# Optimization experiments

Measured on AMD Instinct MI355X. Metric: run time of the kernel, lower is better.

## Reference

```python
import jax, jax.numpy as jnp
import numpy as np

N_HEAD = 16

def setup_inputs() -> dict:
    key = jax.random.key(0)
    ks = jax.random.split(key, 4)
    B, S, E = 2, 2048, 1024
    x = jax.random.normal(ks[0], (B, S, E), dtype=jnp.float32)
    W_qkv = jax.random.normal(ks[1], (E, 3 * E), dtype=jnp.float32) * (1.0 / np.sqrt(E))
    b_qkv = jnp.zeros((3 * E,), dtype=jnp.float32)
    W_proj = jax.random.normal(ks[2], (E, E), dtype=jnp.float32) * (1.0 / np.sqrt(E))
    b_proj = jnp.zeros((E,), dtype=jnp.float32)
    return {"x": x, "W_qkv": W_qkv, "b_qkv": b_qkv, "W_proj": W_proj, "b_proj": b_proj}


def reference(x, W_qkv, b_qkv, W_proj, b_proj):
    B, S, E = x.shape
    H = N_HEAD
    D = E // H
    scale = 1.0 / np.sqrt(D).astype(np.float32)

    qkv = x @ W_qkv + b_qkv                      # [B,S,3E]
    q, k, v = jnp.split(qkv, 3, axis=2)
    # Original code does .view(B, H, S, D) directly (no transpose); replicate exactly.
    q = q.reshape(B, H, S, D)
    k = k.reshape(B, H, S, D)
    v = v.reshape(B, H, S, D)

    att = jnp.einsum('bhqd,bhkd->bhqk', q, k) * scale   # [B,H,S,S]
    causal = jnp.tril(jnp.ones((S, S), dtype=bool))      # True = visible
    att = jnp.where(causal[None, None], att, jnp.float32(-jnp.inf))
    att = jax.nn.softmax(att, axis=-1)
    # dropout is identity in eval mode (p used only at train)
    res = jnp.einsum('bhqk,bhkd->bhqd', att, v)           # [B,H,S,D]
    res = res.transpose(0, 2, 1, 3).reshape(B, S, E)      # matches transpose(1,2).view
    return res @ W_proj + b_proj
```

## Files before the change

### kernel.cpp

```cpp
#include <hip/hip_runtime.h>
#include <hip/hip_bf16.h>

using bf16 = __hip_bfloat16;
using s16x8 = __attribute__((ext_vector_type(8))) short;
using f32x4 = __attribute__((ext_vector_type(4))) float;
typedef unsigned short u16;
typedef unsigned int u32;

#define DEVINL __device__ __forceinline__

DEVINL u16 f2bf(float f) {
  u32 u = __float_as_uint(f);
  u32 r = (u + 0x7fffu + ((u >> 16) & 1u)) >> 16;
  return (u16)r;
}

DEVINL void gload_lds16(const void* g, void* l) {
  __builtin_amdgcn_global_load_lds(
      (__attribute__((address_space(1))) void*)(void*)(g),
      (__attribute__((address_space(3))) void*)(l), 16, 0, 0);
}

__global__ __launch_bounds__(256) void cast_f32_bf16(
    const float* __restrict__ in, bf16* __restrict__ out, int n) {
  int i = (blockIdx.x * 256 + threadIdx.x) * 8;
  float4 a = *(const float4*)(in + i);
  float4 b = *(const float4*)(in + i + 4);
  u16 tmp[8] = {f2bf(a.x), f2bf(a.y), f2bf(a.z), f2bf(a.w),
                f2bf(b.x), f2bf(b.y), f2bf(b.z), f2bf(b.w)};
  *(uint4*)(out + i) = *(const uint4*)tmp;
}

__global__ __launch_bounds__(256) void transpose_cast(
    const float* __restrict__ W, bf16* __restrict__ Wt, int K, int N) {
  __shared__ float tile[64][65];
  int n0 = blockIdx.x * 64, k0 = blockIdx.y * 64;
  int t = threadIdx.x;
#pragma unroll
  for (int i = 0; i < 16; ++i) {
    int idx = i * 256 + t;
    int r = idx >> 6, c = idx & 63;
    tile[r][c] = W[(size_t)(k0 + r) * N + n0 + c];
  }
  __syncthreads();
#pragma unroll
  for (int i = 0; i < 16; ++i) {
    int idx = i * 256 + t;
    int r = idx >> 6, c = idx & 63;
    Wt[(size_t)(n0 + r) * K + k0 + c] = __float2bfloat16(tile[c][r]);
  }
}

template <int MODE>
__global__ __launch_bounds__(256) void gemm_bt(
    const bf16* __restrict__ A, const bf16* __restrict__ Bt,
    const float* __restrict__ bias,
    bf16* __restrict__ q, bf16* __restrict__ k, bf16* __restrict__ v,
    float* __restrict__ outf, int M, int N, int K) {
  __shared__ bf16 As[128 * 64];
  __shared__ bf16 Bs[128 * 64];
  const int tid = threadIdx.x;
  const int w = tid >> 6, lane = tid & 63;
  const int lr = lane >> 4, lc = lane & 15;
  const int wr = w >> 1, wc = w & 1;
  const int m0 = blockIdx.x * 128, n0 = blockIdx.y * 128;

  f32x4 acc[4][4] = {};

  const int srow = lane >> 3;
  const int scolb = ((lane & 7) * 16) ^ (srow << 4);
  const char* Abase = (const char*)(A + (size_t)m0 * K);
  const char* Bbase = (const char*)(Bt + (size_t)n0 * K);
  const int Krow = K * 2;

  for (int kt = 0; kt < K; kt += 64) {
    __syncthreads();
#pragma unroll
    for (int c = 0; c < 4; ++c) {
      int row = w * 32 + c * 8 + srow;
      gload_lds16(Abase + (size_t)row * Krow + kt * 2 + scolb,
                  (char*)As + w * 4096 + c * 1024 + lane * 16);
    }
#pragma unroll
    for (int c = 0; c < 4; ++c) {
      int row = w * 32 + c * 8 + srow;
      gload_lds16(Bbase + (size_t)row * Krow + kt * 2 + scolb,
                  (char*)Bs + w * 4096 + c * 1024 + lane * 16);
    }
    __syncthreads();
#pragma unroll
    for (int ks = 0; ks < 2; ++ks) {
      s16x8 af[4], bfr[4];
#pragma unroll
      for (int mi = 0; mi < 4; ++mi) {
        int row = wr * 64 + mi * 16 + lc;
        int colb = (ks * 64 + lr * 16) ^ ((row & 7) << 4);
        af[mi] = *(const s16x8*)((const char*)As + row * 128 + colb);
      }
#pragma unroll
      for (int ni = 0; ni < 4; ++ni) {
        int row = wc * 64 + ni * 16 + lc;
        int colb = (ks * 64 + lr * 16) ^ ((row & 7) << 4);
        bfr[ni] = *(const s16x8*)((const char*)Bs + row * 128 + colb);
      }
#pragma unroll
      for (int mi = 0; mi < 4; ++mi)
#pragma unroll
        for (int ni = 0; ni < 4; ++ni)
          acc[mi][ni] = __builtin_amdgcn_mfma_f32_16x16x32_bf16(
              af[mi], bfr[ni], acc[mi][ni], 0, 0, 0);
    }
  }

#pragma unroll
  for (int mi = 0; mi < 4; ++mi) {
#pragma unroll
    for (int ni = 0; ni < 4; ++ni) {
      int col = n0 + wc * 64 + ni * 16 + lc;
      float bb = bias[col];
      int rowb = m0 + wr * 64 + mi * 16 + lr * 4;
#pragma unroll
      for (int r = 0; r < 4; ++r) {
        float val = acc[mi][ni][r] + bb;
        int row = rowb + r;
        if (MODE == 0) {
          bf16* o = (col < 1024) ? q : ((col < 2048) ? k : v);
          int cc = col & 1023;
          o[(size_t)row * 1024 + cc] = __float2bfloat16(val);
        } else {
          outf[(size_t)row * N + col] = val;
        }
      }
    }
  }
}

__global__ __launch_bounds__(256) void attn_kernel(
    const bf16* __restrict__ qb, const bf16* __restrict__ kb,
    const bf16* __restrict__ vb, bf16* __restrict__ ob) {
  __shared__ bf16 Ks[64 * 64];
  __shared__ bf16 Vt[64 * 64];
  __shared__ bf16 Ps[128 * 64];

  const int idx = blockIdx.x;
  const int qt = 15 - (idx >> 5);
  const int bh = idx & 31;
  const int b = bh >> 4, h = bh & 15;
  const size_t hb = ((size_t)(b * 2048 + h * 128)) * 1024;
  const bf16* qh = qb + hb;
  const bf16* kh = kb + hb;
  const bf16* vh = vb + hb;

  const int tid = threadIdx.x;
  const int w = tid >> 6, lane = tid & 63;
  const int lr = lane >> 4, lc = lane & 15;

  s16x8 qf[2][2];
#pragma unroll
  for (int mi = 0; mi < 2; ++mi)
#pragma unroll
    for (int ks = 0; ks < 2; ++ks)
      qf[mi][ks] = *(const s16x8*)(qh + (size_t)(qt * 128 + w * 32 + mi * 16 + lc) * 64 +
                                   ks * 32 + lr * 8);

  f32x4 o_acc[2][4] = {};
  float m_run[2][4], l_run[2][4];
#pragma unroll
  for (int mi = 0; mi < 2; ++mi)
#pragma unroll
    for (int r = 0; r < 4; ++r) { m_run[mi][r] = -INFINITY; l_run[mi][r] = 0.f; }

  const int srow = lane >> 3;
  const int scolb = ((lane & 7) * 16) ^ (srow << 4);

  const int nt = (qt + 1) * 2;
  for (int t = 0; t < nt; ++t) {
    __syncthreads();
#pragma unroll
    for (int c = 0; c < 2; ++c) {
      int row = w * 16 + c * 8 + srow;
      gload_lds16((const char*)(kh + (size_t)(t * 64 + row) * 64) + scolb,
                  (char*)Ks + w * 2048 + c * 1024 + lane * 16);
    }
#pragma unroll
    for (int c = 0; c < 2; ++c) {
      int key = lane;
      int d0 = (c * 4 + w) * 8;
      uint4 val = *(const uint4*)(vh + (size_t)(t * 64 + key) * 64 + d0);
      const u16* e = (const u16*)&val;
#pragma unroll
      for (int j = 0; j < 8; ++j) {
        int d = d0 + j;
        *(u16*)((char*)Vt + d * 128 + ((key * 2) ^ ((j & 7) << 4))) = e[j];
      }
    }
    __syncthreads();

    f32x4 s[2][4] = {};
#pragma unroll
    for (int ks = 0; ks < 2; ++ks) {
      s16x8 kf[4];
#pragma unroll
      for (int nj = 0; nj < 4; ++nj) {
        int row = nj * 16 + lc;
        int colb = (ks * 64 + lr * 16) ^ ((row & 7) << 4);
        kf[nj] = *(const s16x8*)((const char*)Ks + row * 128 + colb);
      }
#pragma unroll
      for (int mi = 0; mi < 2; ++mi)
#pragma unroll
        for (int nj = 0; nj < 4; ++nj)
          s[mi][nj] = __builtin_amdgcn_mfma_f32_16x16x32_bf16(
              qf[mi][ks], kf[nj], s[mi][nj], 0, 0, 0);
    }

#pragma unroll
    for (int mi = 0; mi < 2; ++mi) {
#pragma unroll
      for (int r = 0; r < 4; ++r) {
        const int qlocal = w * 32 + mi * 16 + lr * 4 + r;
        const int qg = qt * 128 + qlocal;
        float vv[4];
        float mx = -INFINITY;
#pragma unroll
        for (int nj = 0; nj < 4; ++nj) {
          int kg = t * 64 + nj * 16 + lc;
          float val = s[mi][nj][r] * 0.125f;
          val = (kg <= qg) ? val : -INFINITY;
          vv[nj] = val;
          mx = fmaxf(mx, val);
        }
#pragma unroll
        for (int off = 1; off < 16; off <<= 1) mx = fmaxf(mx, __shfl_xor(mx, off));
        float mold = m_run[mi][r];
        float mnew = fmaxf(mold, mx);
        float sf = __expf(mold - mnew);
        m_run[mi][r] = mnew;
        float ps = 0.f;
#pragma unroll
        for (int nj = 0; nj < 4; ++nj) {
          float p = __expf(vv[nj] - mnew);
          ps += p;
          int key = nj * 16 + lc;
          *(u16*)((char*)Ps + qlocal * 128 + ((key * 2) ^ ((qlocal & 7) << 4))) = f2bf(p);
        }
#pragma unroll
        for (int off = 1; off < 16; off <<= 1) ps += __shfl_xor(ps, off);
        l_run[mi][r] = l_run[mi][r] * sf + ps;
#pragma unroll
        for (int dj = 0; dj < 4; ++dj) o_acc[mi][dj][r] *= sf;
      }
    }

#pragma unroll
    for (int ks = 0; ks < 2; ++ks) {
      s16x8 pf[2], vf[4];
#pragma unroll
      for (int mi = 0; mi < 2; ++mi) {
        int row = w * 32 + mi * 16 + lc;
        int colb = (ks * 64 + lr * 16) ^ ((row & 7) << 4);
        pf[mi] = *(const s16x8*)((const char*)Ps + row * 128 + colb);
      }
#pragma unroll
      for (int dj = 0; dj < 4; ++dj) {
        int row = dj * 16 + lc;
        int colb = (ks * 64 + lr * 16) ^ ((row & 7) << 4);
        vf[dj] = *(const s16x8*)((const char*)Vt + row * 128 + colb);
      }
#pragma unroll
      for (int mi = 0; mi < 2; ++mi)
#pragma unroll
        for (int dj = 0; dj < 4; ++dj)
          o_acc[mi][dj] = __builtin_amdgcn_mfma_f32_16x16x32_bf16(
              pf[mi], vf[dj], o_acc[mi][dj], 0, 0, 0);
    }
  }

#pragma unroll
  for (int mi = 0; mi < 2; ++mi) {
#pragma unroll
    for (int r = 0; r < 4; ++r) {
      float inv = 1.0f / l_run[mi][r];
      int qg = qt * 128 + w * 32 + mi * 16 + lr * 4 + r;
      size_t base = ((size_t)(b * 2048 + qg)) * 1024 + h * 64;
#pragma unroll
      for (int dj = 0; dj < 4; ++dj)
        ob[base + dj * 16 + lc] = __float2bfloat16(o_acc[mi][dj][r] * inv);
    }
  }
}

extern "C" void kernel_launch(void* const* d_in, const int* in_sizes, int n_in,
                              void* d_out, int out_size, void* d_ws, size_t ws_size,
                              hipStream_t stream) {
  const float* x = (const float*)d_in[0];
  const float* Wqkv = (const float*)d_in[1];
  const float* bqkv = (const float*)d_in[2];
  const float* Wproj = (const float*)d_in[3];
  const float* bproj = (const float*)d_in[4];
  float* out = (float*)d_out;

  char* ws = (char*)d_ws;
  bf16* xb = (bf16*)(ws);
  bf16* Wt1 = (bf16*)(ws + 8388608);
  bf16* Wt2 = (bf16*)(ws + 14680064);
  bf16* qb = (bf16*)(ws + 16777216);
  bf16* kb = (bf16*)(ws + 25165824);
  bf16* vb = (bf16*)(ws + 33554432);
  bf16* Ob = xb;

  cast_f32_bf16<<<2048, 256, 0, stream>>>(x, xb, 4096 * 1024);
  transpose_cast<<<dim3(48, 16), 256, 0, stream>>>(Wqkv, Wt1, 1024, 3072);
  transpose_cast<<<dim3(16, 16), 256, 0, stream>>>(Wproj, Wt2, 1024, 1024);
  gemm_bt<0><<<dim3(32, 24), 256, 0, stream>>>(xb, Wt1, bqkv, qb, kb, vb, nullptr,
                                               4096, 3072, 1024);
  attn_kernel<<<512, 256, 0, stream>>>(qb, kb, vb, Ob);
  gemm_bt<1><<<dim3(32, 8), 256, 0, stream>>>(Ob, Wt2, bproj, nullptr, nullptr, nullptr,
                                              out, 4096, 1024, 1024);
}
```

Baseline: 247.9 us.

## Rewrite attention with 32x32 MFMA, register-resident P, and pre-transposed V

```diff
diff --git a/kernel.cpp b/kernel.cpp
--- a/kernel.cpp
+++ b/kernel.cpp
@@ -4,6 +4,7 @@
 using bf16 = __hip_bfloat16;
 using s16x8 = __attribute__((ext_vector_type(8))) short;
 using f32x4 = __attribute__((ext_vector_type(4))) float;
+using f32x16 = __attribute__((ext_vector_type(16))) float;
 typedef unsigned short u16;
 typedef unsigned int u32;
 
@@ -13,6 +14,13 @@
   u32 u = __float_as_uint(f);
   u32 r = (u + 0x7fffu + ((u >> 16) & 1u)) >> 16;
   return (u16)r;
+}
+
+DEVINL u32 pkbf(float a, float b) {
+  __hip_bfloat162 h = __float22bfloat162_rn(make_float2(a, b));
+  union { __hip_bfloat162 h; u32 u; } c;
+  c.h = h;
+  return c.u;
 }
 
 DEVINL void gload_lds16(const void* g, void* l) {
@@ -48,6 +56,34 @@
     int idx = i * 256 + t;
     int r = idx >> 6, c = idx & 63;
     Wt[(size_t)(n0 + r) * K + k0 + c] = __float2bfloat16(tile[c][r]);
+  }
+}
+
+__global__ __launch_bounds__(256) void v_transpose(
+    const bf16* __restrict__ vb, bf16* __restrict__ vt) {
+  __shared__ u16 lt[64][68];
+  const int bh = blockIdx.y;
+  const int s0 = blockIdx.x * 64;
+  const int tid = threadIdx.x;
+  const bf16* src = vb + (size_t)bh * 131072;
+#pragma unroll
+  for (int i = 0; i < 2; ++i) {
+    int c = i * 256 + tid;
+    int srow = c >> 3, sc = (c & 7) * 8;
+    uint4 v = *(const uint4*)(src + (size_t)(s0 + srow) * 64 + sc);
+    const u16* e = (const u16*)&v;
+#pragma unroll
+    for (int j = 0; j < 8; ++j) lt[srow][sc + j] = e[j];
+  }
+  __syncthreads();
+#pragma unroll
+  for (int i = 0; i < 2; ++i) {
+    int c = i * 256 + tid;
+    int drow = c >> 3, sc = (c & 7) * 8;
+    u16 tmp[8];
+#pragma unroll
+    for (int j = 0; j < 8; ++j) tmp[j] = lt[sc + j][drow];
+    *(uint4*)(vt + (size_t)(bh * 64 + drow) * 2048 + s0 + sc) = *(const uint4*)tmp;
   }
 }
 
@@ -124,6 +160,7 @@
         float val = acc[mi][ni][r] + bb;
         int row = rowb + r;
         if (MODE == 0) {
+          if (col < 1024) val *= 0.125f;
           bf16* o = (col < 1024) ? q : ((col < 2048) ? k : v);
           int cc = col & 1023;
           o[(size_t)row * 1024 + cc] = __float2bfloat16(val);
@@ -137,156 +174,144 @@
 
 __global__ __launch_bounds__(256) void attn_kernel(
     const bf16* __restrict__ qb, const bf16* __restrict__ kb,
-    const bf16* __restrict__ vb, bf16* __restrict__ ob) {
-  __shared__ bf16 Ks[64 * 64];
-  __shared__ bf16 Vt[64 * 64];
-  __shared__ bf16 Ps[128 * 64];
-
+    const bf16* __restrict__ vtp, bf16* __restrict__ ob) {
   const int idx = blockIdx.x;
-  const int qt = 15 - (idx >> 5);
-  const int bh = idx & 31;
+  const int bh_lo = idx & 7;
+  const int r0 = idx >> 3;
+  const int bh = ((r0 >> 4) << 3) + bh_lo;
+  const int qbk = 15 - (r0 & 15);
   const int b = bh >> 4, h = bh & 15;
-  const size_t hb = ((size_t)(b * 2048 + h * 128)) * 1024;
+  const int tid = threadIdx.x;
+  const int w = tid >> 6;
+  const int lane = tid & 63;
+  const int l31 = lane & 31;
+  const int hi = lane >> 5;
+
+  const int jj = qbk * 4 + w;
+  const int qbase = jj * 32;
+  const int qg = qbase + l31;
+
+  const size_t hb = (size_t)bh * 131072;
   const bf16* qh = qb + hb;
   const bf16* kh = kb + hb;
-  const bf16* vh = vb + hb;
-
-  const int tid = threadIdx.x;
-  const int w = tid >> 6, lane = tid & 63;
-  const int lr = lane >> 4, lc = lane & 15;
-
-  s16x8 qf[2][2];
-#pragma unroll
-  for (int mi = 0; mi < 2; ++mi)
-#pragma unroll
-    for (int ks = 0; ks < 2; ++ks)
-      qf[mi][ks] = *(const s16x8*)(qh + (size_t)(qt * 128 + w * 32 + mi * 16 + lc) * 64 +
-                                   ks * 32 + lr * 8);
-
-  f32x4 o_acc[2][4] = {};
-  float m_run[2][4], l_run[2][4];
-#pragma unroll
-  for (int mi = 0; mi < 2; ++mi)
-#pragma unroll
-    for (int r = 0; r < 4; ++r) { m_run[mi][r] = -INFINITY; l_run[mi][r] = 0.f; }
-
-  const int srow = lane >> 3;
-  const int scolb = ((lane & 7) * 16) ^ (srow << 4);
-
-  const int nt = (qt + 1) * 2;
+  const bf16* vh = vtp + hb;
+
+  s16x8 qf[4];
+#pragma unroll
+  for (int db = 0; db < 4; ++db)
+    qf[db] = *(const s16x8*)(qh + (size_t)(qbase + l31) * 64 + db * 16 + hi * 8);
+
+  f32x16 o0 = {}, o1 = {};
+  float m_run = -INFINITY, l_run = 0.f;
+  const float LOG2E = 1.44269504f;
+
+  const int nt = (qbase >> 6) + 1;
   for (int t = 0; t < nt; ++t) {
-    __syncthreads();
-#pragma unroll
-    for (int c = 0; c < 2; ++c) {
-      int row = w * 16 + c * 8 + srow;
-      gload_lds16((const char*)(kh + (size_t)(t * 64 + row) * 64) + scolb,
-                  (char*)Ks + w * 2048 + c * 1024 + lane * 16);
-    }
-#pragma unroll
-    for (int c = 0; c < 2; ++c) {
-      int key = lane;
-      int d0 = (c * 4 + w) * 8;
-      uint4 val = *(const uint4*)(vh + (size_t)(t * 64 + key) * 64 + d0);
-      const u16* e = (const u16*)&val;
-#pragma unroll
-      for (int j = 0; j < 8; ++j) {
-        int d = d0 + j;
-        *(u16*)((char*)Vt + d * 128 + ((key * 2) ^ ((j & 7) << 4))) = e[j];
-      }
-    }
-    __syncthreads();
-
-    f32x4 s[2][4] = {};
-#pragma unroll
-    for (int ks = 0; ks < 2; ++ks) {
-      s16x8 kf[4];
-#pragma unroll
-      for (int nj = 0; nj < 4; ++nj) {
-        int row = nj * 16 + lc;
-        int colb = (ks * 64 + lr * 16) ^ ((row & 7) << 4);
-        kf[nj] = *(const s16x8*)((const char*)Ks + row * 128 + colb);
-      }
-#pragma unroll
-      for (int mi = 0; mi < 2; ++mi)
-#pragma unroll
-        for (int nj = 0; nj < 4; ++nj)
-          s[mi][nj] = __builtin_amdgcn_mfma_f32_16x16x32_bf16(
-              qf[mi][ks], kf[nj], s[mi][nj], 0, 0, 0);
-    }
-
-#pragma unroll
-    for (int mi = 0; mi < 2; ++mi) {
-#pragma unroll
-      for (int r = 0; r < 4; ++r) {
-        const int qlocal = w * 32 + mi * 16 + lr * 4 + r;
-        const int qg = qt * 128 + qlocal;
-        float vv[4];
-        float mx = -INFINITY;
-#pragma unroll
-        for (int nj = 0; nj < 4; ++nj) {
-          int kg = t * 64 + nj * 16 + lc;
-          float val = s[mi][nj][r] * 0.125f;
-          val = (kg <= qg) ? val : -INFINITY;
-          vv[nj] = val;
-          mx = fmaxf(mx, val);
-        }
-#pragma unroll
-        for (int off = 1; off < 16; off <<= 1) mx = fmaxf(mx, __shfl_xor(mx, off));
-        float mold = m_run[mi][r];
-        float mnew = fmaxf(mold, mx);
-        float sf = __expf(mold - mnew);
-        m_run[mi][r] = mnew;
-        float ps = 0.f;
-#pragma unroll
-        for (int nj = 0; nj < 4; ++nj) {
-          float p = __expf(vv[nj] - mnew);
-          ps += p;
-          int key = nj * 16 + lc;
-          *(u16*)((char*)Ps + qlocal * 128 + ((key * 2) ^ ((qlocal & 7) << 4))) = f2bf(p);
-        }
-#pragma unroll
-        for (int off = 1; off < 16; off <<= 1) ps += __shfl_xor(ps, off);
-        l_run[mi][r] = l_run[mi][r] * sf + ps;
-#pragma unroll
-        for (int dj = 0; dj < 4; ++dj) o_acc[mi][dj][r] *= sf;
-      }
-    }
-
-#pragma unroll
-    for (int ks = 0; ks < 2; ++ks) {
-      s16x8 pf[2], vf[4];
-#pragma unroll
-      for (int mi = 0; mi < 2; ++mi) {
-        int row = w * 32 + mi * 16 + lc;
-        int colb = (ks * 64 + lr * 16) ^ ((row & 7) << 4);
-        pf[mi] = *(const s16x8*)((const char*)Ps + row * 128 + colb);
-      }
-#pragma unroll
-      for (int dj = 0; dj < 4; ++dj) {
-        int row = dj * 16 + lc;
-        int colb = (ks * 64 + lr * 16) ^ ((row & 7) << 4);
-        vf[dj] = *(const s16x8*)((const char*)Vt + row * 128 + colb);
-      }
-#pragma unroll
-      for (int mi = 0; mi < 2; ++mi)
-#pragma unroll
-        for (int dj = 0; dj < 4; ++dj)
-          o_acc[mi][dj] = __builtin_amdgcn_mfma_f32_16x16x32_bf16(
-              pf[mi], vf[dj], o_acc[mi][dj], 0, 0, 0);
-    }
-  }
-
-#pragma unroll
-  for (int mi = 0; mi < 2; ++mi) {
-#pragma unroll
-    for (int r = 0; r < 4; ++r) {
-      float inv = 1.0f / l_run[mi][r];
-      int qg = qt * 128 + w * 32 + mi * 16 + lr * 4 + r;
-      size_t base = ((size_t)(b * 2048 + qg)) * 1024 + h * 64;
-#pragma unroll
-      for (int dj = 0; dj < 4; ++dj)
-        ob[base + dj * 16 + lc] = __float2bfloat16(o_acc[mi][dj][r] * inv);
-    }
+    f32x16 s0 = {}, s1 = {};
+#pragma unroll
+    for (int db = 0; db < 4; ++db) {
+      s16x8 kf0 = *(const s16x8*)(kh + (size_t)(t * 64 + l31) * 64 + db * 16 + hi * 8);
+      s0 = __builtin_amdgcn_mfma_f32_32x32x16_bf16(kf0, qf[db], s0, 0, 0, 0);
+    }
+#pragma unroll
+    for (int db = 0; db < 4; ++db) {
+      s16x8 kf1 = *(const s16x8*)(kh + (size_t)(t * 64 + 32 + l31) * 64 + db * 16 + hi * 8);
+      s1 = __builtin_amdgcn_mfma_f32_32x32x16_bf16(kf1, qf[db], s1, 0, 0, 0);
+    }
+
+    if (t == nt - 1) {
+#pragma unroll
+      for (int r = 0; r < 16; ++r) {
+        int kvr = t * 64 + (r & 3) + 8 * (r >> 2) + 4 * hi;
+        if (kvr > qg) s0[r] = -INFINITY;
+        if (kvr + 32 > qg) s1[r] = -INFINITY;
+      }
+    }
+
+    float mx[16];
+#pragma unroll
+    for (int r = 0; r < 16; ++r) mx[r] = fmaxf(s0[r], s1[r]);
+#pragma unroll
+    for (int off = 8; off >= 1; off >>= 1)
+#pragma unroll
+      for (int r = 0; r < 8; ++r)
+        if (r < off) mx[r] = fmaxf(mx[r], mx[r + off]);
+    float mxv = fmaxf(mx[0], __shfl_xor(mx[0], 32));
+
+    if (!__all(mxv <= m_run + 8.f)) {
+      float mnew = fmaxf(m_run, mxv);
+      float sf = exp2f((m_run - mnew) * LOG2E);
+      m_run = mnew;
+      l_run *= sf;
+#pragma unroll
+      for (int r = 0; r < 16; ++r) {
+        float sfr = __shfl(sf, (r & 3) + 8 * (r >> 2) + 4 * hi);
+        o0[r] *= sfr;
+        o1[r] *= sfr;
+      }
+    }
+
+    const float nmC = -m_run * LOG2E;
+    float ps[16];
+#pragma unroll
+    for (int r = 0; r < 16; ++r) {
+      float p0 = exp2f(__builtin_fmaf(s0[r], LOG2E, nmC));
+      float p1 = exp2f(__builtin_fmaf(s1[r], LOG2E, nmC));
+      s0[r] = p0;
+      s1[r] = p1;
+      ps[r] = p0 + p1;
+    }
+#pragma unroll
+    for (int off = 8; off >= 1; off >>= 1)
+#pragma unroll
+      for (int r = 0; r < 8; ++r)
+        if (r < off) ps[r] += ps[r + off];
+    l_run += ps[0] + __shfl_xor(ps[0], 32);
+
+    s16x8 vf[4][2];
+#pragma unroll
+    for (int cc = 0; cc < 4; ++cc)
+#pragma unroll
+      for (int ds = 0; ds < 2; ++ds)
+        vf[cc][ds] = *(const s16x8*)(vh + (size_t)(ds * 32 + l31) * 2048 +
+                                     t * 64 + cc * 16 + hi * 8);
+
+    auto mk = [&](float p0, float p1, float p2, float p3,
+                  float p4, float p5, float p6, float p7) -> s16x8 {
+      u32 A0 = pkbf(p0, p1), A1 = pkbf(p2, p3);
+      u32 C0 = pkbf(p4, p5), C1 = pkbf(p6, p7);
+      u32 pA0 = (u32)__shfl_xor((int)A0, 32);
+      u32 pA1 = (u32)__shfl_xor((int)A1, 32);
+      u32 pC0 = (u32)__shfl_xor((int)C0, 32);
+      u32 pC1 = (u32)__shfl_xor((int)C1, 32);
+      union { u32 u[4]; s16x8 v; } f;
+      f.u[0] = hi ? pC0 : A0;
+      f.u[1] = hi ? pC1 : A1;
+      f.u[2] = hi ? C0 : pA0;
+      f.u[3] = hi ? C1 : pA1;
+      return f.v;
+    };
+    s16x8 pa[4];
+    pa[0] = mk(s0[0], s0[1], s0[2], s0[3], s0[4], s0[5], s0[6], s0[7]);
+    pa[1] = mk(s0[8], s0[9], s0[10], s0[11], s0[12], s0[13], s0[14], s0[15]);
+    pa[2] = mk(s1[0], s1[1], s1[2], s1[3], s1[4], s1[5], s1[6], s1[7]);
+    pa[3] = mk(s1[8], s1[9], s1[10], s1[11], s1[12], s1[13], s1[14], s1[15]);
+
+#pragma unroll
+    for (int cc = 0; cc < 4; ++cc) {
+      o0 = __builtin_amdgcn_mfma_f32_32x32x16_bf16(pa[cc], vf[cc][0], o0, 0, 0, 0);
+      o1 = __builtin_amdgcn_mfma_f32_32x32x16_bf16(pa[cc], vf[cc][1], o1, 0, 0, 0);
+    }
+  }
+
+  float inv = 1.f / l_run;
+#pragma unroll
+  for (int r = 0; r < 16; ++r) {
+    int qrow = (r & 3) + 8 * (r >> 2) + 4 * hi;
+    float ivr = __shfl(inv, qrow);
+    bf16* orow = ob + (size_t)(b * 2048 + qbase + qrow) * 1024 + h * 64;
+    orow[l31] = __float2bfloat16(o0[r] * ivr);
+    orow[32 + l31] = __float2bfloat16(o1[r] * ivr);
   }
 }
 
@@ -307,6 +332,7 @@
   bf16* qb = (bf16*)(ws + 16777216);
   bf16* kb = (bf16*)(ws + 25165824);
   bf16* vb = (bf16*)(ws + 33554432);
+  bf16* vtb = (bf16*)(ws + 41943040);
   bf16* Ob = xb;
 
   cast_f32_bf16<<<2048, 256, 0, stream>>>(x, xb, 4096 * 1024);
@@ -314,7 +340,8 @@
   transpose_cast<<<dim3(16, 16), 256, 0, stream>>>(Wproj, Wt2, 1024, 1024);
   gemm_bt<0><<<dim3(32, 24), 256, 0, stream>>>(xb, Wt1, bqkv, qb, kb, vb, nullptr,
                                                4096, 3072, 1024);
-  attn_kernel<<<512, 256, 0, stream>>>(qb, kb, vb, Ob);
+  v_transpose<<<dim3(32, 32), 256, 0, stream>>>(vb, vtb);
+  attn_kernel<<<512, 256, 0, stream>>>(qb, kb, vtb, Ob);
   gemm_bt<1><<<dim3(32, 8), 256, 0, stream>>>(Ob, Wt2, bproj, nullptr, nullptr, nullptr,
                                               out, 4096, 1024, 1024);
 }
```

Measured after the change: 289.2 us. 16.6% more time.
